# Kernel tuning notes

Hardware: AMD Instinct MI355X
Metric: run time of the kernel (lower is better)

Reference implementation:

```python
import jax, jax.numpy as jnp
import numpy as np

NEG_BIG = 1e30  # matches the 1e+30 masking constant in the original


def setup_inputs() -> dict:
    key = jax.random.key(0)
    ks = jax.random.split(key, 6)
    B, Lc, Lq, D = 8, 512, 64, 256
    return {
        "context": jax.random.normal(ks[0], (B, Lc, D), jnp.float32),
        "question": jax.random.normal(ks[1], (B, Lq, D), jnp.float32),
        "mask": jnp.ones((B, Lq), jnp.int32),
        "att_w": jax.random.normal(ks[2], (3 * D,), jnp.float32) * 0.05,  # Linear(6H=3D -> 1) weight
        "att_b": jnp.zeros((1,), jnp.float32),                            # Linear bias
        "w_in": jax.random.normal(ks[3], (D,), jnp.float32) * 0.05,       # input_linear (no bias)
        "w_mem": jax.random.normal(ks[4], (D,), jnp.float32) * 0.05,      # memory_linear (no bias)
    }


def reference(context, question, mask, att_w, att_b, w_in, w_mem):
    # context: [B,Lc,D], question: [B,Lq,D], mask: [B,Lq] (0/1)
    D = context.shape[-1]
    # Separable (mathematically identical) form of Linear(cat([c, q, c*q])):
    # score[b,i,j] = c_i . w_c + q_j . w_q + sum_d c[b,i,d]*q[b,j,d]*w_p[d] + b
    w_c, w_q, w_p = att_w[:D], att_w[D:2 * D], att_w[2 * D:]
    sc = jnp.einsum('bid,d->bi', context, w_c)                 # [B,Lc]
    sq = jnp.einsum('bjd,d->bj', question, w_q)                # [B,Lq]
    sp = jnp.einsum('bid,bjd->bij', context * w_p, question)   # [B,Lc,Lq]
    attention = sc[:, :, None] + sq[:, None, :] + sp + att_b[0]

    maskf = mask.astype(attention.dtype)
    masked = attention - NEG_BIG * (1.0 - maskf)[:, None, :]   # [B,Lc,Lq]

    ctx1 = jnp.einsum('bid,d->bi', context, w_in)[..., None]   # input_linear:  [B,Lc,1]
    q1 = jnp.einsum('bjd,d->bj', question, w_mem)[..., None]   # memory_linear: [B,Lq,1]

    h_aware_weight = jax.nn.softmax(masked, axis=-1)           # [B,Lc,Lq]
    U = jnp.matmul(h_aware_weight, q1)                         # [B,Lc,1]

    u_aware_weight = jax.nn.softmax(jnp.max(masked, axis=-1), axis=-1)[:, None, :]  # [B,1,Lc]
    H = jnp.matmul(u_aware_weight, ctx1)                       # [B,1,1]

    G = jnp.concatenate([ctx1, U, ctx1 * U, U * H], axis=-1)   # [B,Lc,4]
    return G
```

## Files before the change

kernel.cpp:

```cpp
#include <hip/hip_runtime.h>

#define NB 8
#define LC 512
#define LQ 64
#define DD 256
#define NEG_BIG_F 1e30f

#define TPB 256
#define NWAVE 4
#define RPW 4
#define RPB 16
#define BPB (LC / RPB)

__device__ __forceinline__ float bcastf(float x, int lane) {
  return __uint_as_float((unsigned)__builtin_amdgcn_readlane((int)__float_as_uint(x), lane));
}

__global__ __launch_bounds__(TPB) void rows_kernel(
    const float* __restrict__ context,
    const float* __restrict__ question,
    const int*   __restrict__ mask,
    const float* __restrict__ att_w,
    const float* __restrict__ att_b,
    const float* __restrict__ w_in,
    const float* __restrict__ w_mem,
    float4* __restrict__ ws4)
{
  __shared__ float4 qs4[64][64];
  __shared__ float sq_part[LQ][NWAVE + 1];
  __shared__ float q1_part[LQ][NWAVE + 1];
  __shared__ float sqm[LQ];
  __shared__ float q1s[LQ];

  const int tid  = threadIdx.x;
  const int w    = tid >> 6;
  const int l    = tid & 63;
  const int b    = blockIdx.x / BPB;
  const int row0 = (blockIdx.x % BPB) * RPB;
  const int i0   = row0 + w * RPW;

  const float4 wc4 = ((const float4*)att_w)[l];
  const float4 wp4 = ((const float4*)(att_w + 2 * DD))[l];
  const float4 wi4 = ((const float4*)w_in)[l];
  float4 c4r[RPW];
#pragma unroll
  for (int r = 0; r < RPW; ++r)
    c4r[r] = ((const float4*)(context + ((size_t)b * LC + i0 + r) * DD))[l];

  {
    const float4* qrow = (const float4*)(question + ((size_t)b * LQ + l) * DD + w * 64);
    const float4* wqp  = (const float4*)(att_w + DD + w * 64);
    const float4* wmp  = (const float4*)(w_mem + w * 64);
    float psq = 0.f, pq1 = 0.f;
#pragma unroll
    for (int k = 0; k < 16; ++k) {
      float4 v = qrow[k];
      float4 a = wqp[k];
      float4 c = wmp[k];
      psq += v.x*a.x + v.y*a.y + v.z*a.z + v.w*a.w;
      pq1 += v.x*c.x + v.y*c.y + v.z*c.z + v.w*c.w;
      qs4[w * 16 + k][l] = v;
    }
    sq_part[l][w] = psq;
    q1_part[l][w] = pq1;
  }
  __syncthreads();
  if (tid < LQ) {
    const int j = tid;
    float sq = att_b[0];
    float q1 = 0.f;
#pragma unroll
    for (int k = 0; k < NWAVE; ++k) { sq += sq_part[j][k]; q1 += q1_part[j][k]; }
    float mf = (float)mask[b * LQ + j];
    sqm[j] = sq - NEG_BIG_F * (1.0f - mf);
    q1s[j] = q1;
  }
  __syncthreads();

  float4 cp[RPW];
  float sc[RPW], c1[RPW];
#pragma unroll
  for (int r = 0; r < RPW; ++r) {
    float4 c4 = c4r[r];
    sc[r] = c4.x*wc4.x + c4.y*wc4.y + c4.z*wc4.z + c4.w*wc4.w;
    c1[r] = c4.x*wi4.x + c4.y*wi4.y + c4.z*wi4.z + c4.w*wi4.w;
    cp[r].x = c4.x*wp4.x; cp[r].y = c4.y*wp4.y; cp[r].z = c4.z*wp4.z; cp[r].w = c4.w*wp4.w;
  }
#pragma unroll
  for (int off = 32; off > 0; off >>= 1) {
#pragma unroll
    for (int r = 0; r < RPW; ++r) {
      sc[r] += __shfl_xor(sc[r], off);
      c1[r] += __shfl_xor(c1[r], off);
    }
  }

  float acc[RPW] = {0.f, 0.f, 0.f, 0.f};
#pragma unroll
  for (int c = 0; c < 64; ++c) {
    float4 qv = qs4[c][l];
#pragma unroll
    for (int r = 0; r < RPW; ++r) {
      acc[r] += bcastf(cp[r].x, c) * qv.x
              + bcastf(cp[r].y, c) * qv.y
              + bcastf(cp[r].z, c) * qv.z
              + bcastf(cp[r].w, c) * qv.w;
    }
  }

  const float sqm_l = sqm[l];
  const float q1_l  = q1s[l];
#pragma unroll
  for (int r = 0; r < RPW; ++r) {
    float v = acc[r] + sc[r] + sqm_l;
    float m = v;
#pragma unroll
    for (int off = 32; off > 0; off >>= 1) m = fmaxf(m, __shfl_xor(m, off));
    float p  = __expf(v - m);
    float ps = p;
    float pu = p * q1_l;
#pragma unroll
    for (int off = 32; off > 0; off >>= 1) {
      ps += __shfl_xor(ps, off);
      pu += __shfl_xor(pu, off);
    }
    if (l == 0) {
      const int gi = b * LC + i0 + r;
      ws4[gi] = make_float4(m, c1[r], pu / ps, 0.f);
    }
  }
}

__global__ __launch_bounds__(512) void batch_kernel(
    const float4* __restrict__ ws4,
    float4* __restrict__ out4)
{
  const int b  = blockIdx.x;
  const int t  = threadIdx.x;
  const int gi = b * LC + t;
  const float4 v = ws4[gi];
  const float m = v.x, c1 = v.y, U = v.z;

  const int w = t >> 6, l = t & 63;
  __shared__ float rmax[8], rs[8], rc[8];

  float mx = m;
#pragma unroll
  for (int off = 32; off > 0; off >>= 1) mx = fmaxf(mx, __shfl_xor(mx, off));
  if (l == 0) rmax[w] = mx;
  __syncthreads();
  mx = rmax[0];
#pragma unroll
  for (int k = 1; k < 8; ++k) mx = fmaxf(mx, rmax[k]);

  float p  = __expf(m - mx);
  float ps = p;
  float pc = p * c1;
#pragma unroll
  for (int off = 32; off > 0; off >>= 1) {
    ps += __shfl_xor(ps, off);
    pc += __shfl_xor(pc, off);
  }
  if (l == 0) { rs[w] = ps; rc[w] = pc; }
  __syncthreads();
  float S = 0.f, C = 0.f;
#pragma unroll
  for (int k = 0; k < 8; ++k) { S += rs[k]; C += rc[k]; }

  const float H = C / S;
  out4[gi] = make_float4(c1, U, c1 * U, U * H);
}

extern "C" void kernel_launch(void* const* d_in, const int* in_sizes, int n_in,
                              void* d_out, int out_size, void* d_ws, size_t ws_size,
                              hipStream_t stream) {
  const float* context  = (const float*)d_in[0];
  const float* question = (const float*)d_in[1];
  const int*   mask     = (const int*)d_in[2];
  const float* att_w    = (const float*)d_in[3];
  const float* att_b    = (const float*)d_in[4];
  const float* w_in     = (const float*)d_in[5];
  const float* w_mem    = (const float*)d_in[6];
  float4* out4 = (float4*)d_out;
  float4* ws4  = (float4*)d_ws;

  rows_kernel<<<dim3(NB * BPB), dim3(TPB), 0, stream>>>(
      context, question, mask, att_w, att_b, w_in, w_mem, ws4);
  batch_kernel<<<dim3(NB), dim3(512), 0, stream>>>(ws4, out4);
}
```

Baseline: 85.06 us.

## Use one row per wave, transpose question tile in LDS with XOR swizzle

The rows kernel now uses 512 threads (8 waves) with one context row per wave instead of four. The question tile is stored transposed in shared memory with an XOR swizzle so the inner product reads it without bank conflicts. The sq and q1 projections are now computed by wave-level shuffle reductions, which removes one block barrier and the partial-sum arrays. Each block reuses the question tile for only half as many rows, so the grid doubles and question loads into LDS double. Having fewer rows per wave may lower register pressure and raise occupancy.

```diff
diff --git a/kernel.cpp b/kernel.cpp
--- a/kernel.cpp
+++ b/kernel.cpp
@@ -6,17 +6,16 @@
 #define DD 256
 #define NEG_BIG_F 1e30f
 
-#define TPB 256
-#define NWAVE 4
-#define RPW 4
-#define RPB 16
+#define TPB 512
+#define NWAVE 8
+#define RPB 8
 #define BPB (LC / RPB)
 
 __device__ __forceinline__ float bcastf(float x, int lane) {
   return __uint_as_float((unsigned)__builtin_amdgcn_readlane((int)__float_as_uint(x), lane));
 }
 
-__global__ __launch_bounds__(TPB) void rows_kernel(
+__global__ __launch_bounds__(TPB, 4) void rows_kernel(
     const float* __restrict__ context,
     const float* __restrict__ question,
     const int*   __restrict__ mask,
@@ -26,109 +25,94 @@
     const float* __restrict__ w_mem,
     float4* __restrict__ ws4)
 {
-  __shared__ float4 qs4[64][64];
-  __shared__ float sq_part[LQ][NWAVE + 1];
-  __shared__ float q1_part[LQ][NWAVE + 1];
-  __shared__ float sqm[LQ];
-  __shared__ float q1s[LQ];
+  __shared__ float4 T[64][64];
+  __shared__ float sq_raw[LQ];
+  __shared__ float q1_s[LQ];
 
   const int tid  = threadIdx.x;
   const int w    = tid >> 6;
   const int l    = tid & 63;
   const int b    = blockIdx.x / BPB;
   const int row0 = (blockIdx.x % BPB) * RPB;
-  const int i0   = row0 + w * RPW;
+  const int i    = row0 + w;
 
   const float4 wc4 = ((const float4*)att_w)[l];
+  const float4 wq4 = ((const float4*)(att_w + DD))[l];
   const float4 wp4 = ((const float4*)(att_w + 2 * DD))[l];
   const float4 wi4 = ((const float4*)w_in)[l];
-  float4 c4r[RPW];
+  const float4 wm4 = ((const float4*)w_mem)[l];
+  const float4 c4  = ((const float4*)(context + ((size_t)b * LC + i) * DD))[l];
+
+  float4 v[8];
 #pragma unroll
-  for (int r = 0; r < RPW; ++r)
-    c4r[r] = ((const float4*)(context + ((size_t)b * LC + i0 + r) * DD))[l];
+  for (int k = 0; k < 8; ++k)
+    v[k] = ((const float4*)(question + ((size_t)b * LQ + (k * 8 + w)) * DD))[l];
+#pragma unroll
+  for (int k = 0; k < 8; ++k)
+    T[l][(k * 8 + w) ^ (l & 7)] = v[k];
 
-  {
-    const float4* qrow = (const float4*)(question + ((size_t)b * LQ + l) * DD + w * 64);
-    const float4* wqp  = (const float4*)(att_w + DD + w * 64);
-    const float4* wmp  = (const float4*)(w_mem + w * 64);
-    float psq = 0.f, pq1 = 0.f;
+  float psq[8], pq1[8];
 #pragma unroll
-    for (int k = 0; k < 16; ++k) {
-      float4 v = qrow[k];
-      float4 a = wqp[k];
-      float4 c = wmp[k];
-      psq += v.x*a.x + v.y*a.y + v.z*a.z + v.w*a.w;
-      pq1 += v.x*c.x + v.y*c.y + v.z*c.z + v.w*c.w;
-      qs4[w * 16 + k][l] = v;
-    }
-    sq_part[l][w] = psq;
-    q1_part[l][w] = pq1;
-  }
-  __syncthreads();
-  if (tid < LQ) {
-    const int j = tid;
-    float sq = att_b[0];
-    float q1 = 0.f;
-#pragma unroll
-    for (int k = 0; k < NWAVE; ++k) { sq += sq_part[j][k]; q1 += q1_part[j][k]; }
-    float mf = (float)mask[b * LQ + j];
-    sqm[j] = sq - NEG_BIG_F * (1.0f - mf);
-    q1s[j] = q1;
-  }
-  __syncthreads();
-
-  float4 cp[RPW];
-  float sc[RPW], c1[RPW];
-#pragma unroll
-  for (int r = 0; r < RPW; ++r) {
-    float4 c4 = c4r[r];
-    sc[r] = c4.x*wc4.x + c4.y*wc4.y + c4.z*wc4.z + c4.w*wc4.w;
-    c1[r] = c4.x*wi4.x + c4.y*wi4.y + c4.z*wi4.z + c4.w*wi4.w;
-    cp[r].x = c4.x*wp4.x; cp[r].y = c4.y*wp4.y; cp[r].z = c4.z*wp4.z; cp[r].w = c4.w*wp4.w;
+  for (int k = 0; k < 8; ++k) {
+    psq[k] = v[k].x*wq4.x + v[k].y*wq4.y + v[k].z*wq4.z + v[k].w*wq4.w;
+    pq1[k] = v[k].x*wm4.x + v[k].y*wm4.y + v[k].z*wm4.z + v[k].w*wm4.w;
   }
 #pragma unroll
   for (int off = 32; off > 0; off >>= 1) {
 #pragma unroll
-    for (int r = 0; r < RPW; ++r) {
-      sc[r] += __shfl_xor(sc[r], off);
-      c1[r] += __shfl_xor(c1[r], off);
+    for (int k = 0; k < 8; ++k) {
+      psq[k] += __shfl_xor(psq[k], off);
+      pq1[k] += __shfl_xor(pq1[k], off);
+    }
+  }
+  if (l == 0) {
+#pragma unroll
+    for (int k = 0; k < 8; ++k) {
+      sq_raw[k * 8 + w] = psq[k];
+      q1_s[k * 8 + w]   = pq1[k];
     }
   }
 
-  float acc[RPW] = {0.f, 0.f, 0.f, 0.f};
+  float4 cp;
+  cp.x = c4.x*wp4.x; cp.y = c4.y*wp4.y; cp.z = c4.z*wp4.z; cp.w = c4.w*wp4.w;
+  float sc = c4.x*wc4.x + c4.y*wc4.y + c4.z*wc4.z + c4.w*wc4.w;
+  float c1 = c4.x*wi4.x + c4.y*wi4.y + c4.z*wi4.z + c4.w*wi4.w;
+#pragma unroll
+  for (int off = 32; off > 0; off >>= 1) {
+    sc += __shfl_xor(sc, off);
+    c1 += __shfl_xor(c1, off);
+  }
+
+  __syncthreads();
+
+  float a0 = 0.f, a1 = 0.f, a2 = 0.f, a3 = 0.f;
 #pragma unroll
   for (int c = 0; c < 64; ++c) {
-    float4 qv = qs4[c][l];
-#pragma unroll
-    for (int r = 0; r < RPW; ++r) {
-      acc[r] += bcastf(cp[r].x, c) * qv.x
-              + bcastf(cp[r].y, c) * qv.y
-              + bcastf(cp[r].z, c) * qv.z
-              + bcastf(cp[r].w, c) * qv.w;
-    }
+    float4 qv = T[c][l ^ (c & 7)];
+    a0 += bcastf(cp.x, c) * qv.x;
+    a1 += bcastf(cp.y, c) * qv.y;
+    a2 += bcastf(cp.z, c) * qv.z;
+    a3 += bcastf(cp.w, c) * qv.w;
   }
 
-  const float sqm_l = sqm[l];
-  const float q1_l  = q1s[l];
+  const float mf = (float)mask[b * LQ + l];
+  const float vscore = (a0 + a1) + (a2 + a3) + sc + sq_raw[l] + att_b[0]
+                       - NEG_BIG_F * (1.0f - mf);
+  const float q1_l = q1_s[l];
+
+  float m = vscore;
 #pragma unroll
-  for (int r = 0; r < RPW; ++r) {
-    float v = acc[r] + sc[r] + sqm_l;
-    float m = v;
+  for (int off = 32; off > 0; off >>= 1) m = fmaxf(m, __shfl_xor(m, off));
+  float p  = __expf(vscore - m);
+  float ps = p;
+  float pu = p * q1_l;
 #pragma unroll
-    for (int off = 32; off > 0; off >>= 1) m = fmaxf(m, __shfl_xor(m, off));
-    float p  = __expf(v - m);
-    float ps = p;
-    float pu = p * q1_l;
-#pragma unroll
-    for (int off = 32; off > 0; off >>= 1) {
-      ps += __shfl_xor(ps, off);
-      pu += __shfl_xor(pu, off);
-    }
-    if (l == 0) {
-      const int gi = b * LC + i0 + r;
-      ws4[gi] = make_float4(m, c1[r], pu / ps, 0.f);
-    }
+  for (int off = 32; off > 0; off >>= 1) {
+    ps += __shfl_xor(ps, off);
+    pu += __shfl_xor(pu, off);
   }
+  if (l == 0)
+    ws4[b * LC + i] = make_float4(m, c1, pu / ps, 0.f);
 }
 
 __global__ __launch_bounds__(512) void batch_kernel(
```

Result: faster. 77.50 us (median of 2 runs) (-8.9%).
